# Performance work log

Hardware: AMD Instinct MI355X
Metric: run time of the kernel (lower is better)

Reference implementation:

```python
import jax, jax.numpy as jnp
import numpy as np

N = 50000
E = 1600000
F_IN = 128
C_OUT = 64
HEADS = 2
NEG_SLOPE = 0.2
EPS = 1e-5


def setup_inputs() -> dict:
    key = jax.random.key(0)
    ks = jax.random.split(key, 8)
    HC = HEADS * C_OUT
    glorot = lambda k, shape: jax.random.normal(k, shape, jnp.float32) * np.sqrt(2.0 / (shape[0] + shape[-1]))
    return {
        "x": jax.random.normal(ks[0], (N, F_IN), jnp.float32),
        "edge_index": jax.random.randint(ks[1], (2, E), 0, N, jnp.int64),
        "W_l": glorot(ks[2], (F_IN, HC)),
        "W_r": glorot(ks[3], (F_IN, HC)),
        "att": glorot(ks[4], (HEADS, C_OUT)),
        "bias": jnp.zeros((HC,), jnp.float32),
        "gn_weight": jnp.ones((HC,), jnp.float32),
        "gn_bias": jnp.zeros((HC,), jnp.float32),
        "gn_mean_scale": jnp.ones((HC,), jnp.float32),
    }


def reference(x, edge_index, W_l, W_r, att, bias, gn_weight, gn_bias, gn_mean_scale):
    n = x.shape[0]
    # --- GATv2Conv (share_weights=False, concat=True, dropout=0) ---
    x_l = (x @ W_l).reshape(n, HEADS, C_OUT)  # source transform
    x_r = (x @ W_r).reshape(n, HEADS, C_OUT)  # target transform
    # add self loops
    loop = jnp.arange(n, dtype=edge_index.dtype)
    src = jnp.concatenate([edge_index[0], loop])
    dst = jnp.concatenate([edge_index[1], loop])
    # edge-wise attention logits: LeakyReLU(x_l[j] + x_r[i]) . att
    xs = x_l[src] + x_r[dst]  # [E', H, C]
    e = jax.nn.leaky_relu(xs, NEG_SLOPE)
    logits = jnp.einsum('ehc,hc->eh', e, att)  # [E', H]
    # segment softmax over edges sharing the same target node
    seg_max = jax.ops.segment_max(logits, dst, num_segments=n)  # [N, H]
    exp = jnp.exp(logits - seg_max[dst])
    seg_sum = jax.ops.segment_sum(exp, dst, num_segments=n)
    alpha = exp / seg_sum[dst]  # [E', H]
    # scatter-aggregate messages
    msg = alpha[:, :, None] * x_l[src]  # [E', H, C]
    out = jax.ops.segment_sum(msg, dst, num_segments=n)  # [N, H, C]
    out = out.reshape(n, HEADS * C_OUT) + bias
    # --- GraphNorm (single graph) ---
    mean = out.mean(axis=0)
    centered = out - mean * gn_mean_scale
    var = (centered * centered).mean(axis=0)
    return gn_weight * centered / jnp.sqrt(var + EPS) + gn_bias
```

## Files before the change

### kernel.cpp

```cpp
#include <hip/hip_runtime.h>
#include <math.h>

#define NEG_SLOPE 0.2f
#define GN_EPS 1e-5f
#define NBSHIFT 8
#define CHUNK 8192

typedef _Float16 h2 __attribute__((ext_vector_type(2)));
typedef _Float16 half8 __attribute__((ext_vector_type(8)));
typedef float f32x4 __attribute__((ext_vector_type(4)));

__device__ __forceinline__ int rfl(int v) {
  return __builtin_amdgcn_readfirstlane(v);
}

__device__ __forceinline__ unsigned int pkh(float a, float b) {
  return __builtin_bit_cast(unsigned int, __builtin_amdgcn_cvt_pkrtz(a, b));
}

__device__ __forceinline__ h2 bch2(unsigned int u) {
  return __builtin_bit_cast(h2, u);
}

__device__ __forceinline__ h2 mkh2(float a, float b) {
  return __builtin_bit_cast(h2, __builtin_amdgcn_cvt_pkrtz(a, b));
}

__device__ __forceinline__ float dot2f(h2 a, h2 b, float c) {
#if __has_builtin(__builtin_amdgcn_fdot2)
  return __builtin_amdgcn_fdot2(a, b, c, false);
#else
  return fmaf((float)a.x, (float)b.x, fmaf((float)a.y, (float)b.y, c));
#endif
}

__device__ __forceinline__ float lkdot(h2 xl, h2 xr, h2 a, float p) {
  h2 t = xl + xr;
  h2 z = {(_Float16)0.f, (_Float16)0.f};
#if __has_builtin(__builtin_elementwise_min)
  h2 mn = __builtin_elementwise_min(t, z);
#else
  h2 mn;
  mn.x = (t.x < z.x) ? t.x : z.x;
  mn.y = (t.y < z.y) ? t.y : z.y;
#endif
  h2 km1 = {(_Float16)(NEG_SLOPE - 1.0f), (_Float16)(NEG_SLOPE - 1.0f)};
  h2 g = mn * km1 + t;
  return dot2f(g, a, p);
}

__global__ __launch_bounds__(256) void gemm_hist(
    const float* __restrict__ x, const float* __restrict__ Wl,
    const float* __restrict__ Wr, unsigned int* __restrict__ xlb,
    unsigned int* __restrict__ xrh, int n, const int* __restrict__ ei,
    int* __restrict__ bhist, int e, int gemm_blocks) {
  if ((int)blockIdx.x >= gemm_blocks) {
    __shared__ int hist[256];
    hist[threadIdx.x] = 0;
    __syncthreads();
    const int nbk = gridDim.x - gemm_blocks;
    const int stride = nbk * 256;
    for (int i = ((int)blockIdx.x - gemm_blocks) * 256 + threadIdx.x; i < e;
         i += stride)
      atomicAdd(&hist[ei[e + i] >> NBSHIFT], 1);
    __syncthreads();
    int v = hist[threadIdx.x];
    if (v > 0) atomicAdd(&bhist[threadIdx.x], v);
    return;
  }

  const int wv = threadIdx.x >> 6;
  const int lane = threadIdx.x & 63;
  const int lr = lane & 15;
  const int lk = lane >> 4;
  const int node0 = (int)blockIdx.x * 64;
  const float* __restrict__ Wp = (wv < 2) ? Wl : Wr;
  unsigned int* __restrict__ dst = (wv < 2) ? xlb : xrh;
  const int chBase = (wv & 1) * 64;

  f32x4 acc[4][4];
#pragma unroll
  for (int mt = 0; mt < 4; ++mt)
#pragma unroll
    for (int nt = 0; nt < 4; ++nt) acc[mt][nt] = (f32x4){0.f, 0.f, 0.f, 0.f};

  int nd[4];
#pragma unroll
  for (int nt = 0; nt < 4; ++nt) nd[nt] = min(node0 + nt * 16 + lr, n - 1);

#pragma unroll
  for (int kc = 0; kc < 4; ++kc) {
    const int k0 = kc * 32 + lk * 8;
    half8 a[4];
#pragma unroll
    for (int mt = 0; mt < 4; ++mt) {
      const float* __restrict__ wp =
          Wp + (size_t)k0 * 128 + chBase + mt * 16 + lr;
      float w0 = wp[0 * 128], w1 = wp[1 * 128], w2 = wp[2 * 128],
            w3 = wp[3 * 128];
      float w4 = wp[4 * 128], w5 = wp[5 * 128], w6 = wp[6 * 128],
            w7 = wp[7 * 128];
      uint4 ua;
      ua.x = pkh(w0, w1);
      ua.y = pkh(w2, w3);
      ua.z = pkh(w4, w5);
      ua.w = pkh(w6, w7);
      a[mt] = __builtin_bit_cast(half8, ua);
    }
    half8 b[4];
#pragma unroll
    for (int nt = 0; nt < 4; ++nt) {
      const float4 f0 = *(const float4*)(x + (size_t)nd[nt] * 128 + k0);
      const float4 f1 = *(const float4*)(x + (size_t)nd[nt] * 128 + k0 + 4);
      uint4 ub;
      ub.x = pkh(f0.x, f0.y);
      ub.y = pkh(f0.z, f0.w);
      ub.z = pkh(f1.x, f1.y);
      ub.w = pkh(f1.z, f1.w);
      b[nt] = __builtin_bit_cast(half8, ub);
    }
#pragma unroll
    for (int mt = 0; mt < 4; ++mt)
#pragma unroll
      for (int nt = 0; nt < 4; ++nt)
        acc[mt][nt] = __builtin_amdgcn_mfma_f32_16x16x32_f16(
            a[mt], b[nt], acc[mt][nt], 0, 0, 0);
  }

  const int dw0 = (chBase >> 1) + lk * 2;
#pragma unroll
  for (int nt = 0; nt < 4; ++nt) {
    const int node = node0 + nt * 16 + lr;
    if (node >= n) continue;
#pragma unroll
    for (int mt = 0; mt < 4; ++mt) {
      uint2 p;
      p.x = pkh(acc[mt][nt][0], acc[mt][nt][1]);
      p.y = pkh(acc[mt][nt][2], acc[mt][nt][3]);
      *(uint2*)(dst + (size_t)node * 64 + dw0 + mt * 8) = p;
    }
  }
}

__global__ __launch_bounds__(256) void bscan(const int* __restrict__ bhist,
                                             int* __restrict__ bbase,
                                             int* __restrict__ gcur,
                                             int* __restrict__ offsets, int nb,
                                             int n, int e) {
  __shared__ int sd[256];
  int t = threadIdx.x;
  int v = (t < nb) ? bhist[t] : 0;
  sd[t] = v;
  __syncthreads();
#pragma unroll
  for (int s = 1; s < 256; s <<= 1) {
    int add = (t >= s) ? sd[t - s] : 0;
    __syncthreads();
    sd[t] += add;
    __syncthreads();
  }
  int excl = sd[t] - v;
  if (t < nb) {
    bbase[t] = excl;
    gcur[t] = excl;
  } else {
    gcur[t] = 0;
  }
  if (t == 0) {
    bbase[nb] = e;
    offsets[n] = e;
  }
}

__global__ __launch_bounds__(256) void partition(const int* __restrict__ ei,
                                                 int* __restrict__ gcur,
                                                 unsigned int* __restrict__ ebuf,
                                                 int e) {
  __shared__ int hist[256];
  __shared__ int lcur[256];
  const int t = threadIdx.x;
  const int c0 = blockIdx.x * CHUNK;
  const int cend = min(c0 + CHUNK, e);
  hist[t] = 0;
  __syncthreads();
  for (int i = c0 + t; i < cend; i += 256)
    atomicAdd(&hist[ei[e + i] >> NBSHIFT], 1);
  __syncthreads();
  lcur[t] = atomicAdd(&gcur[t], hist[t]);
  __syncthreads();
  for (int i = c0 + t; i < cend; i += 256) {
    int dst = ei[e + i];
    int src = ei[i];
    int b = dst >> NBSHIFT;
    int pos = atomicAdd(&lcur[b], 1);
    ebuf[pos] = (unsigned int)src | ((unsigned int)(dst & 255) << 16);
  }
}

__global__ __launch_bounds__(256) void csr_build(
    const unsigned int* __restrict__ ebuf, const int* __restrict__ bbase,
    int* __restrict__ offsets, int* __restrict__ csr_src, int n) {
  __shared__ int hist[256];
  __shared__ int sc[256];
  const int b = blockIdx.x;
  const int t = threadIdx.x;
  const int node0 = b << NBSHIFT;
  const int seg0 = bbase[b];
  const int seg1 = bbase[b + 1];

  hist[t] = 0;
  __syncthreads();
  for (int i = seg0 + t; i < seg1; i += 256)
    atomicAdd(&hist[(ebuf[i] >> 16) & 255], 1);
  __syncthreads();
  int v = hist[t];
  sc[t] = v;
  __syncthreads();
#pragma unroll
  for (int s = 1; s < 256; s <<= 1) {
    int add = (t >= s) ? sc[t - s] : 0;
    __syncthreads();
    sc[t] += add;
    __syncthreads();
  }
  int start = seg0 + sc[t] - v;
  int node = node0 + t;
  if (node < n) offsets[node] = start;
  __syncthreads();
  hist[t] = start;
  __syncthreads();
  for (int i = seg0 + t; i < seg1; i += 256) {
    unsigned int u = ebuf[i];
    int pos = atomicAdd(&hist[(u >> 16) & 255], 1);
    csr_src[pos] = (int)(u & 0xFFFFu);
  }
}

__global__ __launch_bounds__(256) void node_agg(
    const unsigned int* __restrict__ xlh, const unsigned int* __restrict__ xrh,
    const int* __restrict__ offsets, const int* __restrict__ csr_src,
    const float* __restrict__ att, const float* __restrict__ bias,
    float* __restrict__ out, int n) {
  const int wave = threadIdx.x >> 6;
  const int lane = threadIdx.x & 63;
  const int node = blockIdx.x * 4 + wave;
  if (node >= n) return;
  const int q = lane >> 4;
  const int r = lane & 15;

  const uint4 xr4 = *(const uint4*)(xrh + (size_t)node * 64 + r * 4);
  const h2 xr0 = bch2(xr4.x), xr1 = bch2(xr4.y), xr2v = bch2(xr4.z),
           xr3 = bch2(xr4.w);
  const float4 a0 = *(const float4*)(att + r * 8);
  const float4 a1 = *(const float4*)(att + r * 8 + 4);
  const h2 ah0 = mkh2(a0.x, a0.y), ah1 = mkh2(a0.z, a0.w),
           ah2 = mkh2(a1.x, a1.y), ah3 = mkh2(a1.z, a1.w);

  const int start = rfl(offsets[node]);
  const int end = rfl(offsets[node + 1]);
  const int deg = end - start;
  const int T = deg + 1;

  float s = 0.f;
  float accf[8];
#pragma unroll
  for (int i = 0; i < 8; ++i) accf[i] = 0.f;

  const unsigned int* __restrict__ xlp = xlh + r * 4;

  auto quad = [&](int src, bool valid) {
    const uint4 xl4 = *(const uint4*)(xlp + (size_t)src * 64);
    const h2 x0 = bch2(xl4.x), x1 = bch2(xl4.y), x2 = bch2(xl4.z),
             x3 = bch2(xl4.w);
    float p = 0.f;
    p = lkdot(x0, xr0, ah0, p);
    p = lkdot(x1, xr1, ah1, p);
    p = lkdot(x2, xr2v, ah2, p);
    p = lkdot(x3, xr3, ah3, p);
    p += __shfl_xor(p, 1, 64);
    p += __shfl_xor(p, 2, 64);
    p += __shfl_xor(p, 4, 64);
    const float w = valid ? __expf(p) : 0.f;
    s += w;
    accf[0] = fmaf((float)x0.x, w, accf[0]);
    accf[1] = fmaf((float)x0.y, w, accf[1]);
    accf[2] = fmaf((float)x1.x, w, accf[2]);
    accf[3] = fmaf((float)x1.y, w, accf[3]);
    accf[4] = fmaf((float)x2.x, w, accf[4]);
    accf[5] = fmaf((float)x2.y, w, accf[5]);
    accf[6] = fmaf((float)x3.x, w, accf[6]);
    accf[7] = fmaf((float)x3.y, w, accf[7]);
  };

  for (int b0 = 0; b0 < T; b0 += 64) {
    const int m = min(64, T - b0);
    const int kk = b0 + lane;
    const int cl = min(kk, T - 1);
    int idx = node;
    if (deg > 0) {
      idx = csr_src[start + max(cl - 1, 0)];
      if (cl == 0) idx = node;
    }
    int j = 0;
#pragma unroll 2
    for (; j + 4 <= m; j += 4)
      quad(__shfl(idx, j + q, 64), true);
    if (j < m) {
      const int eo = j + q;
      quad(__shfl(idx, min(eo, m - 1), 64), eo < m);
    }
  }

  s += __shfl_xor(s, 16, 64);
  s += __shfl_xor(s, 32, 64);
#pragma unroll
  for (int i = 0; i < 8; ++i) {
    accf[i] += __shfl_xor(accf[i], 16, 64);
    accf[i] += __shfl_xor(accf[i], 32, 64);
  }

  if (q == 0) {
    const float inv = 1.f / s;
    const float4 b0v = *(const float4*)(bias + r * 8);
    const float4 b1v = *(const float4*)(bias + r * 8 + 4);
    float4 o0 = make_float4(fmaf(accf[0], inv, b0v.x), fmaf(accf[1], inv, b0v.y),
                            fmaf(accf[2], inv, b0v.z), fmaf(accf[3], inv, b0v.w));
    float4 o1 = make_float4(fmaf(accf[4], inv, b1v.x), fmaf(accf[5], inv, b1v.y),
                            fmaf(accf[6], inv, b1v.z), fmaf(accf[7], inv, b1v.w));
    *(float4*)(out + (size_t)node * 128 + r * 8) = o0;
    *(float4*)(out + (size_t)node * 128 + r * 8 + 4) = o1;
  }
}

__global__ __launch_bounds__(256) void gn_partial(const float* __restrict__ out,
                                                  float* __restrict__ part,
                                                  int total) {
  float s = 0.f, q = 0.f;
  const int stride = gridDim.x * 256;
  for (int idx = blockIdx.x * 256 + threadIdx.x; idx < total; idx += stride) {
    float v = out[idx];
    s += v;
    q = fmaf(v, v, q);
  }
  __shared__ float sd[256], qd[256];
  sd[threadIdx.x] = s;
  qd[threadIdx.x] = q;
  __syncthreads();
  if (threadIdx.x < 128) {
    part[blockIdx.x * 256 + threadIdx.x] = sd[threadIdx.x] + sd[threadIdx.x + 128];
    part[blockIdx.x * 256 + 128 + threadIdx.x] =
        qd[threadIdx.x] + qd[threadIdx.x + 128];
  }
}

__global__ __launch_bounds__(1024) void gn_final(const float* __restrict__ part,
                                                 const float* __restrict__ gw,
                                                 const float* __restrict__ gb,
                                                 const float* __restrict__ gms,
                                                 float* __restrict__ AB,
                                                 int nblocks, float inv_n) {
  __shared__ float sS[8][128];
  __shared__ float sQ[8][128];
  const int c = threadIdx.x & 127;
  const int sl = threadIdx.x >> 7;
  float S = 0.f, Q = 0.f;
#pragma unroll 4
  for (int b = sl; b < nblocks; b += 8) {
    S += part[b * 256 + c];
    Q += part[b * 256 + 128 + c];
  }
  sS[sl][c] = S;
  sQ[sl][c] = Q;
  __syncthreads();
  if (sl == 0) {
#pragma unroll
    for (int i = 1; i < 8; ++i) {
      S += sS[i][c];
      Q += sQ[i][c];
    }
    float mean = S * inv_n;
    float msc = mean * gms[c];
    float var = Q * inv_n - 2.f * msc * mean + msc * msc;
    float scale = gw[c] * rsqrtf(var + GN_EPS);
    AB[c] = scale;
    AB[128 + c] = gb[c] - scale * msc;
  }
}

__global__ void gn_apply(float* __restrict__ out, const float* __restrict__ AB,
                         int total4) {
  int i = blockIdx.x * blockDim.x + threadIdx.x;
  if (i >= total4) return;
  float4 v = ((float4*)out)[i];
  int c4 = (i & 31) * 4;
  v.x = fmaf(AB[c4 + 0], v.x, AB[128 + c4 + 0]);
  v.y = fmaf(AB[c4 + 1], v.y, AB[128 + c4 + 1]);
  v.z = fmaf(AB[c4 + 2], v.z, AB[128 + c4 + 2]);
  v.w = fmaf(AB[c4 + 3], v.w, AB[128 + c4 + 3]);
  ((float4*)out)[i] = v;
}

extern "C" void kernel_launch(void* const* d_in, const int* in_sizes, int n_in,
                              void* d_out, int out_size, void* d_ws,
                              size_t ws_size, hipStream_t stream) {
  const float* x = (const float*)d_in[0];
  const int* ei = (const int*)d_in[1];
  const float* Wl = (const float*)d_in[2];
  const float* Wr = (const float*)d_in[3];
  const float* att = (const float*)d_in[4];
  const float* bias = (const float*)d_in[5];
  const float* gw = (const float*)d_in[6];
  const float* gb = (const float*)d_in[7];
  const float* gms = (const float*)d_in[8];
  float* out = (float*)d_out;

  const int n = in_sizes[0] / 128;
  const int e = in_sizes[1] / 2;
  const int nb = (n + 255) >> NBSHIFT;
  const int nchunks = (e + CHUNK - 1) / CHUNK;
  const int GN_BLOCKS = 256;
  const int gemm_blocks = (n + 63) / 64;
  const int hist_blocks = 196;

  char* w = (char*)d_ws;
  auto alloc = [&](size_t bytes) {
    char* p = w;
    w += (bytes + 255) & ~(size_t)255;
    return p;
  };
  unsigned int* xlb = (unsigned int*)alloc((size_t)n * 64 * sizeof(int));
  unsigned int* xrh = (unsigned int*)alloc((size_t)n * 64 * sizeof(int));
  int* offsets = (int*)alloc((size_t)(n + 1) * sizeof(int));
  int* csr_src = (int*)alloc((size_t)e * sizeof(int));
  unsigned int* ebuf = (unsigned int*)alloc((size_t)e * sizeof(int));
  int* bhist = (int*)alloc(256 * sizeof(int));
  int* bbase = (int*)alloc((size_t)(nb + 1) * sizeof(int));
  int* gcur = (int*)alloc(256 * sizeof(int));
  float* part = (float*)alloc((size_t)GN_BLOCKS * 256 * sizeof(float));
  float* AB = (float*)alloc(256 * sizeof(float));

  hipMemsetAsync(bhist, 0, 256 * sizeof(int), stream);

  gemm_hist<<<gemm_blocks + hist_blocks, 256, 0, stream>>>(
      x, Wl, Wr, xlb, xrh, n, ei, bhist, e, gemm_blocks);
  bscan<<<1, 256, 0, stream>>>(bhist, bbase, gcur, offsets, nb, n, e);
  partition<<<nchunks, 256, 0, stream>>>(ei, gcur, ebuf, e);
  csr_build<<<nb, 256, 0, stream>>>(ebuf, bbase, offsets, csr_src, n);
  node_agg<<<(n + 3) / 4, 256, 0, stream>>>(xlb, xrh, offsets, csr_src, att,
                                            bias, out, n);
  gn_partial<<<GN_BLOCKS, 256, 0, stream>>>(out, part, n * 128);
  gn_final<<<1, 1024, 0, stream>>>(part, gw, gb, gms, AB, GN_BLOCKS,
                                   1.0f / (float)n);
  gn_apply<<<(n * 32 + 255) / 256, 256, 0, stream>>>(out, AB, n * 32);
}
```

Measured before the change: 270.0 us.

## Retune partition chunking, widen csr_build blocks, vectorize GraphNorm partial reduction

Several independent tweaks land together. The partition chunk size shrinks so more blocks run, and csr_build moves to 1024-thread blocks while keeping the 256-wide scan. node_agg now computes gather addresses with 32-bit shift/or arithmetic, and gn_partial reads float4 with a per-column shared-memory reduction over twice as many blocks. Smaller chunks add more global cursor atomics, and the address arithmetic assumes the xl buffer offset fits in 32 bits.

```diff
diff --git a/kernel.cpp b/kernel.cpp
--- a/kernel.cpp
+++ b/kernel.cpp
@@ -4,7 +4,7 @@
 #define NEG_SLOPE 0.2f
 #define GN_EPS 1e-5f
 #define NBSHIFT 8
-#define CHUNK 8192
+#define CHUNK 2048
 
 typedef _Float16 h2 __attribute__((ext_vector_type(2)));
 typedef _Float16 half8 __attribute__((ext_vector_type(8)));
@@ -197,7 +197,7 @@
   }
 }
 
-__global__ __launch_bounds__(256) void csr_build(
+__global__ __launch_bounds__(1024) void csr_build(
     const unsigned int* __restrict__ ebuf, const int* __restrict__ bbase,
     int* __restrict__ offsets, int* __restrict__ csr_src, int n) {
   __shared__ int hist[256];
@@ -208,28 +208,32 @@
   const int seg0 = bbase[b];
   const int seg1 = bbase[b + 1];
 
-  hist[t] = 0;
-  __syncthreads();
-  for (int i = seg0 + t; i < seg1; i += 256)
+  if (t < 256) hist[t] = 0;
+  __syncthreads();
+  for (int i = seg0 + t; i < seg1; i += 1024)
     atomicAdd(&hist[(ebuf[i] >> 16) & 255], 1);
   __syncthreads();
-  int v = hist[t];
-  sc[t] = v;
+  int v = 0;
+  if (t < 256) {
+    v = hist[t];
+    sc[t] = v;
+  }
   __syncthreads();
 #pragma unroll
   for (int s = 1; s < 256; s <<= 1) {
-    int add = (t >= s) ? sc[t - s] : 0;
-    __syncthreads();
-    sc[t] += add;
-    __syncthreads();
-  }
-  int start = seg0 + sc[t] - v;
-  int node = node0 + t;
-  if (node < n) offsets[node] = start;
-  __syncthreads();
-  hist[t] = start;
-  __syncthreads();
-  for (int i = seg0 + t; i < seg1; i += 256) {
+    int add = (t >= s && t < 256) ? sc[t - s] : 0;
+    __syncthreads();
+    if (t < 256) sc[t] += add;
+    __syncthreads();
+  }
+  if (t < 256) {
+    int start = seg0 + sc[t] - v;
+    int node = node0 + t;
+    if (node < n) offsets[node] = start;
+    hist[t] = start;
+  }
+  __syncthreads();
+  for (int i = seg0 + t; i < seg1; i += 1024) {
     unsigned int u = ebuf[i];
     int pos = atomicAdd(&hist[(u >> 16) & 255], 1);
     csr_src[pos] = (int)(u & 0xFFFFu);
@@ -266,10 +270,12 @@
 #pragma unroll
   for (int i = 0; i < 8; ++i) accf[i] = 0.f;
 
-  const unsigned int* __restrict__ xlp = xlh + r * 4;
+  const char* __restrict__ xlbase = (const char*)xlh;
+  const unsigned roff = (unsigned)(r * 16);
 
   auto quad = [&](int src, bool valid) {
-    const uint4 xl4 = *(const uint4*)(xlp + (size_t)src * 64);
+    const uint4 xl4 =
+        *(const uint4*)(xlbase + (((unsigned)src << 8) | roff));
     const h2 x0 = bch2(xl4.x), x1 = bch2(xl4.y), x2 = bch2(xl4.z),
              x3 = bch2(xl4.w);
     float p = 0.f;
@@ -332,24 +338,39 @@
   }
 }
 
-__global__ __launch_bounds__(256) void gn_partial(const float* __restrict__ out,
+__global__ __launch_bounds__(256) void gn_partial(const float4* __restrict__ out4,
                                                   float* __restrict__ part,
-                                                  int total) {
-  float s = 0.f, q = 0.f;
+                                                  int total4) {
+  const int t = threadIdx.x;
+  float s0 = 0.f, s1 = 0.f, s2 = 0.f, s3 = 0.f;
+  float q0 = 0.f, q1 = 0.f, q2 = 0.f, q3 = 0.f;
   const int stride = gridDim.x * 256;
-  for (int idx = blockIdx.x * 256 + threadIdx.x; idx < total; idx += stride) {
-    float v = out[idx];
-    s += v;
-    q = fmaf(v, v, q);
-  }
-  __shared__ float sd[256], qd[256];
-  sd[threadIdx.x] = s;
-  qd[threadIdx.x] = q;
-  __syncthreads();
-  if (threadIdx.x < 128) {
-    part[blockIdx.x * 256 + threadIdx.x] = sd[threadIdx.x] + sd[threadIdx.x + 128];
-    part[blockIdx.x * 256 + 128 + threadIdx.x] =
-        qd[threadIdx.x] + qd[threadIdx.x + 128];
+  for (int i = blockIdx.x * 256 + t; i < total4; i += stride) {
+    float4 v = out4[i];
+    s0 += v.x; q0 = fmaf(v.x, v.x, q0);
+    s1 += v.y; q1 = fmaf(v.y, v.y, q1);
+    s2 += v.z; q2 = fmaf(v.z, v.z, q2);
+    s3 += v.w; q3 = fmaf(v.w, v.w, q3);
+  }
+  __shared__ float red[8][128];
+  const int row = t >> 5;
+  const int cb = (t & 31) * 4;
+  *(float4*)&red[row][cb] = make_float4(s0, s1, s2, s3);
+  __syncthreads();
+  if (t < 128) {
+    float S = 0.f;
+#pragma unroll
+    for (int r = 0; r < 8; ++r) S += red[r][t];
+    part[blockIdx.x * 256 + t] = S;
+  }
+  __syncthreads();
+  *(float4*)&red[row][cb] = make_float4(q0, q1, q2, q3);
+  __syncthreads();
+  if (t < 128) {
+    float Q = 0.f;
+#pragma unroll
+    for (int r = 0; r < 8; ++r) Q += red[r][t];
+    part[blockIdx.x * 256 + 128 + t] = Q;
   }
 }
 
@@ -364,7 +385,7 @@
   const int c = threadIdx.x & 127;
   const int sl = threadIdx.x >> 7;
   float S = 0.f, Q = 0.f;
-#pragma unroll 4
+#pragma unroll 8
   for (int b = sl; b < nblocks; b += 8) {
     S += part[b * 256 + c];
     Q += part[b * 256 + 128 + c];
@@ -418,7 +439,7 @@
   const int e = in_sizes[1] / 2;
   const int nb = (n + 255) >> NBSHIFT;
   const int nchunks = (e + CHUNK - 1) / CHUNK;
-  const int GN_BLOCKS = 256;
+  const int GN_BLOCKS = 512;
   const int gemm_blocks = (n + 63) / 64;
   const int hist_blocks = 196;
 
@@ -445,10 +466,10 @@
       x, Wl, Wr, xlb, xrh, n, ei, bhist, e, gemm_blocks);
   bscan<<<1, 256, 0, stream>>>(bhist, bbase, gcur, offsets, nb, n, e);
   partition<<<nchunks, 256, 0, stream>>>(ei, gcur, ebuf, e);
-  csr_build<<<nb, 256, 0, stream>>>(ebuf, bbase, offsets, csr_src, n);
+  csr_build<<<nb, 1024, 0, stream>>>(ebuf, bbase, offsets, csr_src, n);
   node_agg<<<(n + 3) / 4, 256, 0, stream>>>(xlb, xrh, offsets, csr_src, att,
                                             bias, out, n);
-  gn_partial<<<GN_BLOCKS, 256, 0, stream>>>(out, part, n * 128);
+  gn_partial<<<GN_BLOCKS, 256, 0, stream>>>((const float4*)out, part, n * 32);
   gn_final<<<1, 1024, 0, stream>>>(part, gw, gb, gms, AB, GN_BLOCKS,
                                    1.0f / (float)n);
   gn_apply<<<(n * 32 + 255) / 256, 256, 0, stream>>>(out, AB, n * 32);
```

Result: faster. 241.3 us (-10.6%).
